# Kernel optimization log

Hardware: AMD Instinct MI355X
Metric: run time of the kernel (lower is better)

## Reference

```python
import jax, jax.numpy as jnp
import numpy as np

B, H, W, C = 2, 256, 256, 96
NH, WS, SS = 3, 8, 4
HD = C // NH
N = WS * WS              # tokens per window
NWIMG = (H // WS) * (W // WS)  # windows per image
MLP = 4 * C
EPS = 1e-5

def _np_attn_mask():
    img = np.zeros((H, W))
    sl = (slice(0, -WS), slice(-WS, -SS), slice(-SS, None))
    cnt = 0
    for a in sl:
        for b in sl:
            img[a, b] = cnt
            cnt += 1
    m = img.reshape(H // WS, WS, W // WS, WS).transpose(0, 2, 1, 3).reshape(-1, N)
    am = m[:, None, :] - m[:, :, None]
    return np.where(am != 0, -100.0, 0.0).astype(np.float32)

def _np_rel_index():
    coords = np.stack(np.meshgrid(np.arange(WS), np.arange(WS), indexing='ij'))
    cf = coords.reshape(2, -1)
    rel = (cf[:, :, None] - cf[:, None, :]).transpose(1, 2, 0).copy()
    rel[..., 0] += WS - 1
    rel[..., 1] += WS - 1
    rel[..., 0] *= 2 * WS - 1
    return rel.sum(-1)

def _np_coords_table():
    r = np.arange(-(WS - 1), WS, dtype=np.float32)
    t = np.stack(np.meshgrid(r, r, indexing='ij'), axis=-1) / (WS - 1) * 8.0
    t = np.sign(t) * np.log2(np.abs(t) + 1.0) / np.log2(8.0)
    return t.reshape(-1, 2)

ATTN_MASK = jnp.asarray(_np_attn_mask())          # [NWIMG, N, N]
REL_INDEX = jnp.asarray(_np_rel_index().reshape(-1))
COORDS_TABLE = jnp.asarray(_np_coords_table())    # [(2WS-1)^2, 2]

def setup_inputs():
    key = jax.random.key(0)
    ks = jax.random.split(key, 16)
    s = 0.02
    return {
        'hidden_states': jax.random.normal(ks[0], (B, H * W, C), jnp.float32),
        'time': jax.random.uniform(ks[1], (B,), jnp.float32),
        'q_w': jax.random.normal(ks[2], (C, C), jnp.float32) * s,
        'q_b': jnp.zeros((C,), jnp.float32),
        'k_w': jax.random.normal(ks[3], (C, C), jnp.float32) * s,
        'v_w': jax.random.normal(ks[4], (C, C), jnp.float32) * s,
        'v_b': jnp.zeros((C,), jnp.float32),
        'proj_w': jax.random.normal(ks[5], (C, C), jnp.float32) * s,
        'proj_b': jnp.zeros((C,), jnp.float32),
        'logit_scale': jnp.full((NH, 1, 1), jnp.log(10.0), jnp.float32),
        'cpb_w1': jax.random.normal(ks[6], (2, 512), jnp.float32) * s,
        'cpb_b1': jnp.zeros((512,), jnp.float32),
        'cpb_w2': jax.random.normal(ks[7], (512, NH), jnp.float32) * s,
        'lnb_ww': jax.random.normal(ks[8], (1, C), jnp.float32) * s,
        'lnb_wb': jnp.ones((C,), jnp.float32),
        'lnb_bw': jax.random.normal(ks[9], (1, C), jnp.float32) * s,
        'lnb_bb': jnp.zeros((C,), jnp.float32),
        'lna_ww': jax.random.normal(ks[10], (1, C), jnp.float32) * s,
        'lna_wb': jnp.ones((C,), jnp.float32),
        'lna_bw': jax.random.normal(ks[11], (1, C), jnp.float32) * s,
        'lna_bb': jnp.zeros((C,), jnp.float32),
        'fc1_w': jax.random.normal(ks[12], (C, MLP), jnp.float32) * s,
        'fc1_b': jnp.zeros((MLP,), jnp.float32),
        'fc2_w': jax.random.normal(ks[13], (MLP, C), jnp.float32) * s,
        'fc2_b': jnp.zeros((C,), jnp.float32),
    }

def _cln(x, time, ww, wb, bw, bb):
    # ConditionalLayerNorm: stats over channels, affine params from time via Linear(1, C)
    mean = x.mean(-1, keepdims=True)
    var = (x * x).mean(-1, keepdims=True) - mean * mean
    xn = (x - mean) / jnp.sqrt(var + EPS)
    t = time.reshape(-1, 1)
    w = (t @ ww + wb)[:, None, :]
    b = (t @ bw + bb)[:, None, :]
    return w * xn + b

def reference(hidden_states, time, q_w, q_b, k_w, v_w, v_b, proj_w, proj_b, logit_scale, cpb_w1, cpb_b1, cpb_w2, lnb_ww, lnb_wb, lnb_bw, lnb_bb, lna_ww, lna_wb, lna_bw, lna_bb, fc1_w, fc1_b, fc2_w, fc2_b):
    shortcut = hidden_states
    x = hidden_states.reshape(B, H, W, C)
    x = jnp.roll(x, (-SS, -SS), axis=(1, 2))  # cyclic shift
    # window partition -> [nW, N, C]
    xw = x.reshape(B, H // WS, WS, W // WS, WS, C).transpose(0, 1, 3, 2, 4, 5).reshape(-1, N, C)
    nW = B * NWIMG
    q = (xw @ q_w + q_b).reshape(nW, N, NH, HD).transpose(0, 2, 1, 3)
    k = (xw @ k_w).reshape(nW, N, NH, HD).transpose(0, 2, 1, 3)  # key has no bias in Swinv2
    v = (xw @ v_w + v_b).reshape(nW, N, NH, HD).transpose(0, 2, 1, 3)
    # cosine attention with clamped learnable log temperature
    qn = q / jnp.maximum(jnp.linalg.norm(q, axis=-1, keepdims=True), 1e-12)
    kn = k / jnp.maximum(jnp.linalg.norm(k, axis=-1, keepdims=True), 1e-12)
    scale = jnp.exp(jnp.minimum(logit_scale, jnp.log(100.0)))  # [NH,1,1]
    attn = jnp.einsum('whnd,whmd->whnm', qn, kn) * scale[None]
    # continuous relative position bias: MLP(2->512->NH) over log-spaced coords
    bias_table = jax.nn.relu(COORDS_TABLE @ cpb_w1 + cpb_b1) @ cpb_w2
    bias = bias_table[REL_INDEX].reshape(N, N, NH).transpose(2, 0, 1)
    attn = attn + 16.0 * jax.nn.sigmoid(bias)[None]
    # shifted-window mask
    attn = attn.reshape(B, NWIMG, NH, N, N) + ATTN_MASK[None, :, None]
    attn = jax.nn.softmax(attn.reshape(nW, NH, N, N), axis=-1)
    ctx = jnp.einsum('whnm,whmd->whnd', attn, v).transpose(0, 2, 1, 3).reshape(nW, N, C)
    ctx = ctx @ proj_w + proj_b
    # window reverse + un-shift
    xr = ctx.reshape(B, H // WS, W // WS, WS, WS, C).transpose(0, 1, 3, 2, 4, 5).reshape(B, H, W, C)
    xr = jnp.roll(xr, (SS, SS), axis=(1, 2))
    attn_out = xr.reshape(B, H * W, C)
    # post-norm residual (Swin v2 style) with conditional LN
    hs = shortcut + _cln(attn_out, time, lnb_ww, lnb_wb, lnb_bw, lnb_bb)
    inter = jax.nn.gelu(hs @ fc1_w + fc1_b, approximate=False)
    mlp_out = inter @ fc2_w + fc2_b
    return hs + _cln(mlp_out, time, lna_ww, lna_wb, lna_bw, lna_bb)
```

## Files before the change

kernel.cpp:

```cpp
#include <hip/hip_runtime.h>
#include <hip/hip_bf16.h>

typedef __bf16 bf16_t;
typedef bf16_t bf16x8 __attribute__((ext_vector_type(8)));
typedef bf16_t bf16x4 __attribute__((ext_vector_type(4)));
typedef float  f32x4  __attribute__((ext_vector_type(4)));

#define LDC 104
#define LDT 72
#define LDP 70
#define LDG 392

#define WS_WQ    0
#define WS_WK    19968
#define WS_WV    39936
#define WS_WP    59904
#define WS_FC1   79872
#define WS_FC2   159744
#define WS_BIAS  235008
#define WS_TBL   284160

__device__ __forceinline__ f32x4 mfma16(bf16x8 a, bf16x8 b, f32x4 c) {
    return __builtin_amdgcn_mfma_f32_16x16x32_bf16(a, b, c, 0, 0, 0);
}

__device__ __forceinline__ float cpbf(int v) {
    float x = (float)v * (8.0f / 7.0f);
    float l = log2f(fabsf(x) + 1.0f) * (1.0f / 3.0f);
    return x < 0.f ? -l : l;
}

__device__ __forceinline__ int regcnt(int t, int hw, int ww) {
    int r = t >> 3, c = t & 7;
    int rr = (hw == 31) ? (r < 4 ? 1 : 2) : 0;
    int cc = (ww == 31) ? (c < 4 ? 1 : 2) : 0;
    return rr * 3 + cc;
}

__global__ __launch_bounds__(256) void k0a_cpb(
    const float* __restrict__ cw1, const float* __restrict__ cb1,
    const float* __restrict__ cw2, char* __restrict__ ws)
{
    const int wv = threadIdx.x >> 6, lane = threadIdx.x & 63;
    const int e = blockIdx.x * 4 + wv;
    if (e >= 225) return;
    int ia = e / 15, ib = e % 15;
    float c0 = cpbf(ia - 7), c1 = cpbf(ib - 7);
    float a0 = 0.f, a1 = 0.f, a2 = 0.f;
    #pragma unroll
    for (int c = 0; c < 8; ++c) {
        int j = c * 64 + lane;
        float h = fmaf(c0, cw1[j], fmaf(c1, cw1[512 + j], cb1[j]));
        h = fmaxf(h, 0.f);
        a0 = fmaf(h, cw2[j * 3 + 0], a0);
        a1 = fmaf(h, cw2[j * 3 + 1], a1);
        a2 = fmaf(h, cw2[j * 3 + 2], a2);
    }
    #pragma unroll
    for (int m = 1; m < 64; m <<= 1) {
        a0 += __shfl_xor(a0, m);
        a1 += __shfl_xor(a1, m);
        a2 += __shfl_xor(a2, m);
    }
    if (lane == 0) {
        float* tbl = (float*)(ws + WS_TBL);
        tbl[e * 3 + 0] = a0; tbl[e * 3 + 1] = a1; tbl[e * 3 + 2] = a2;
    }
}

__global__ __launch_bounds__(512) void k0w_prep(
    const float* __restrict__ qw, const float* __restrict__ kw,
    const float* __restrict__ vw, const float* __restrict__ pw,
    const float* __restrict__ fc1w, const float* __restrict__ fc2w,
    char* __restrict__ ws)
{
    int tid = threadIdx.x;
    if (blockIdx.x < 54) {
        int rid = blockIdx.x * 512 + tid;
        if (rid < 9216) {
            int which = rid / 2304, r = rid % 2304;
            int i = r / 24, o4 = r % 24;
            const float* src = which == 0 ? qw : which == 1 ? kw : which == 2 ? vw : pw;
            float4 u = *(const float4*)(src + i * 96 + 4 * o4);
            bf16_t* dst = (bf16_t*)(ws + WS_WQ + which * 19968);
            dst[(4 * o4 + 0) * LDC + i] = (bf16_t)u.x;
            dst[(4 * o4 + 1) * LDC + i] = (bf16_t)u.y;
            dst[(4 * o4 + 2) * LDC + i] = (bf16_t)u.z;
            dst[(4 * o4 + 3) * LDC + i] = (bf16_t)u.w;
        } else if (rid < 18432) {
            int r = rid - 9216;
            int i = r / 96, m4 = r % 96;
            float4 u = *(const float4*)(fc1w + i * 384 + 4 * m4);
            bf16_t* dst = (bf16_t*)(ws + WS_FC1);
            dst[(4 * m4 + 0) * LDC + i] = (bf16_t)u.x;
            dst[(4 * m4 + 1) * LDC + i] = (bf16_t)u.y;
            dst[(4 * m4 + 2) * LDC + i] = (bf16_t)u.z;
            dst[(4 * m4 + 3) * LDC + i] = (bf16_t)u.w;
        } else {
            int r = rid - 18432;
            int g = r / 24, o4 = r % 24;
            float4 u = *(const float4*)(fc2w + g * 96 + 4 * o4);
            bf16_t* dst = (bf16_t*)(ws + WS_FC2);
            dst[(4 * o4 + 0) * LDG + g] = (bf16_t)u.x;
            dst[(4 * o4 + 1) * LDG + g] = (bf16_t)u.y;
            dst[(4 * o4 + 2) * LDG + g] = (bf16_t)u.z;
            dst[(4 * o4 + 3) * LDG + g] = (bf16_t)u.w;
        }
    } else {
        int e = (blockIdx.x - 54) * 512 + tid;
        if (e < 12288) {
            const float* tbl = (const float*)(ws + WS_TBL);
            float* bias = (float*)(ws + WS_BIAS);
            int h = e >> 12, nm = e & 4095, n = nm >> 6, m = nm & 63;
            int dr = (n >> 3) - (m >> 3) + 7, dc = (n & 7) - (m & 7) + 7;
            float t = tbl[(dr * 15 + dc) * 3 + h];
            bias[e] = 16.f / (1.f + __expf(-t));
        }
    }
}

__global__ __launch_bounds__(256, 3) void kA_attn(
    const float* __restrict__ hidden, const float* __restrict__ tv,
    const float* __restrict__ qb, const float* __restrict__ vb,
    const float* __restrict__ pb, const float* __restrict__ lsc,
    const float* __restrict__ lnww, const float* __restrict__ lnwb,
    const float* __restrict__ lnbw, const float* __restrict__ lnbb,
    const char* __restrict__ ws, float* __restrict__ hs)
{
    __shared__ __align__(16) char sm[40704];
    bf16_t* vT   = (bf16_t*)(sm + 0);
    bf16_t* qn   = (bf16_t*)(sm + 13824);
    bf16_t* kn   = (bf16_t*)(sm + 27136);
    bf16_t* P    = (bf16_t*)(sm + 13824);
    bf16_t* ctxb = (bf16_t*)(sm + 0);

    const int tid = threadIdx.x;
    const int wv = tid >> 6, lane = tid & 63, lg = lane >> 4, lr = lane & 15;
    const int wid = blockIdx.x;
    const int bat = wid >> 10, wim = wid & 1023, hw = wim >> 5, wwi = wim & 31;

    {
        bf16x8 af[3];
        {
            int tok = 16 * wv + lr;
            int gr = ((hw << 3) + (tok >> 3) + 4) & 255;
            int gc = ((wwi << 3) + (tok & 7) + 4) & 255;
            const float* xb = hidden + (((size_t)bat << 16) + (gr << 8) + gc) * 96;
            #pragma unroll
            for (int ks = 0; ks < 3; ++ks) {
                float4 u0 = *(const float4*)(xb + 32 * ks + 8 * lg);
                float4 u1 = *(const float4*)(xb + 32 * ks + 8 * lg + 4);
                bf16x8 f;
                f[0] = (bf16_t)u0.x; f[1] = (bf16_t)u0.y; f[2] = (bf16_t)u0.z; f[3] = (bf16_t)u0.w;
                f[4] = (bf16_t)u1.x; f[5] = (bf16_t)u1.y; f[6] = (bf16_t)u1.z; f[7] = (bf16_t)u1.w;
                af[ks] = f;
            }
        }
        const bf16_t* Wq = (const bf16_t*)(ws + WS_WQ);
        const bf16_t* Wk = (const bf16_t*)(ws + WS_WK);
        const bf16_t* Wv = (const bf16_t*)(ws + WS_WV);

        {
            bf16x8 wf[6][3];
            #pragma unroll
            for (int n = 0; n < 6; ++n)
                #pragma unroll
                for (int ks = 0; ks < 3; ++ks)
                    wf[n][ks] = *(const bf16x8*)(Wq + (16 * n + lr) * LDC + 32 * ks + 8 * lg);
            f32x4 acc[6];
            #pragma unroll
            for (int n = 0; n < 6; ++n) {
                f32x4 a = {0.f,0.f,0.f,0.f};
                #pragma unroll
                for (int ks = 0; ks < 3; ++ks) a = mfma16(af[ks], wf[n][ks], a);
                float bq = qb[16 * n + lr];
                #pragma unroll
                for (int j = 0; j < 4; ++j) a[j] += bq;
                acc[n] = a;
            }
            #pragma unroll
            for (int h = 0; h < 3; ++h)
                #pragma unroll
                for (int j = 0; j < 4; ++j) {
                    float s = acc[2*h][j] * acc[2*h][j] + acc[2*h+1][j] * acc[2*h+1][j];
                    s += __shfl_xor(s, 1); s += __shfl_xor(s, 2); s += __shfl_xor(s, 4); s += __shfl_xor(s, 8);
                    float inv = 1.f / fmaxf(sqrtf(s), 1e-12f);
                    int row = 16 * wv + 4 * lg + j;
                    qn[row * LDC + 32 * h + lr]      = (bf16_t)(acc[2*h][j] * inv);
                    qn[row * LDC + 32 * h + 16 + lr] = (bf16_t)(acc[2*h+1][j] * inv);
                }
        }
        {
            bf16x8 wf[6][3];
            #pragma unroll
            for (int n = 0; n < 6; ++n)
                #pragma unroll
                for (int ks = 0; ks < 3; ++ks)
                    wf[n][ks] = *(const bf16x8*)(Wk + (16 * n + lr) * LDC + 32 * ks + 8 * lg);
            f32x4 acc[6];
            #pragma unroll
            for (int n = 0; n < 6; ++n) {
                f32x4 a = {0.f,0.f,0.f,0.f};
                #pragma unroll
                for (int ks = 0; ks < 3; ++ks) a = mfma16(af[ks], wf[n][ks], a);
                acc[n] = a;
            }
            #pragma unroll
            for (int h = 0; h < 3; ++h)
                #pragma unroll
                for (int j = 0; j < 4; ++j) {
                    float s = acc[2*h][j] * acc[2*h][j] + acc[2*h+1][j] * acc[2*h+1][j];
                    s += __shfl_xor(s, 1); s += __shfl_xor(s, 2); s += __shfl_xor(s, 4); s += __shfl_xor(s, 8);
                    float inv = 1.f / fmaxf(sqrtf(s), 1e-12f);
                    int row = 16 * wv + 4 * lg + j;
                    kn[row * LDC + 32 * h + lr]      = (bf16_t)(acc[2*h][j] * inv);
                    kn[row * LDC + 32 * h + 16 + lr] = (bf16_t)(acc[2*h+1][j] * inv);
                }
        }
        {
            bf16x8 wf[6][3];
            #pragma unroll
            for (int n = 0; n < 6; ++n)
                #pragma unroll
                for (int ks = 0; ks < 3; ++ks)
                    wf[n][ks] = *(const bf16x8*)(Wv + (16 * n + lr) * LDC + 32 * ks + 8 * lg);
            #pragma unroll
            for (int n = 0; n < 6; ++n) {
                f32x4 a = {0.f,0.f,0.f,0.f};
                #pragma unroll
                for (int ks = 0; ks < 3; ++ks) a = mfma16(af[ks], wf[n][ks], a);
                float bv_ = vb[16 * n + lr];
                bf16x4 pk;
                #pragma unroll
                for (int j = 0; j < 4; ++j) pk[j] = (bf16_t)(a[j] + bv_);
                *(bf16x4*)(vT + (16 * n + lr) * LDT + 16 * wv + 4 * lg) = pk;
            }
        }
    }
    __syncthreads();

    {
        float br[3][4][4];
        const float* biasT = (const float*)(ws + WS_BIAS);
        #pragma unroll
        for (int h = 0; h < 3; ++h)
            #pragma unroll
            for (int f = 0; f < 4; ++f)
                #pragma unroll
                for (int j = 0; j < 4; ++j)
                    br[h][f][j] = biasT[(h << 12) + (16 * wv + 4 * lg + j) * 64 + 16 * f + lr];

        f32x4 s[3][4];
        #pragma unroll
        for (int h = 0; h < 3; ++h) {
            bf16x8 aq = *(const bf16x8*)(qn + (16 * wv + lr) * LDC + 32 * h + 8 * lg);
            bf16x8 bk[4];
            #pragma unroll
            for (int f = 0; f < 4; ++f)
                bk[f] = *(const bf16x8*)(kn + (16 * f + lr) * LDC + 32 * h + 8 * lg);
            #pragma unroll
            for (int f = 0; f < 4; ++f) {
                f32x4 z = {0.f,0.f,0.f,0.f};
                s[h][f] = mfma16(aq, bk[f], z);
            }
        }
        __syncthreads();

        float ls[3];
        #pragma unroll
        for (int h = 0; h < 3; ++h) ls[h] = __expf(fminf(lsc[h], 4.6051702f));
        int cntm[4], cnti[4];
        #pragma unroll
        for (int f = 0; f < 4; ++f) cntm[f] = regcnt(16 * f + lr, hw, wwi);
        #pragma unroll
        for (int j = 0; j < 4; ++j) cnti[j] = regcnt(16 * wv + 4 * lg + j, hw, wwi);
        #pragma unroll
        for (int h = 0; h < 3; ++h) {
            #pragma unroll
            for (int f = 0; f < 4; ++f)
                #pragma unroll
                for (int j = 0; j < 4; ++j) {
                    float mk = (cnti[j] != cntm[f]) ? -100.f : 0.f;
                    s[h][f][j] = fmaf(s[h][f][j], ls[h], br[h][f][j] + mk);
                }
            #pragma unroll
            for (int j = 0; j < 4; ++j) {
                float mx = fmaxf(fmaxf(s[h][0][j], s[h][1][j]), fmaxf(s[h][2][j], s[h][3][j]));
                mx = fmaxf(mx, __shfl_xor(mx, 1)); mx = fmaxf(mx, __shfl_xor(mx, 2));
                mx = fmaxf(mx, __shfl_xor(mx, 4)); mx = fmaxf(mx, __shfl_xor(mx, 8));
                float sum = 0.f;
                #pragma unroll
                for (int f = 0; f < 4; ++f) { float e = __expf(s[h][f][j] - mx); s[h][f][j] = e; sum += e; }
                sum += __shfl_xor(sum, 1); sum += __shfl_xor(sum, 2); sum += __shfl_xor(sum, 4); sum += __shfl_xor(sum, 8);
                float inv = 1.f / sum;
                int row = 16 * wv + 4 * lg + j;
                #pragma unroll
                for (int f = 0; f < 4; ++f)
                    P[h * 64 * LDP + row * LDP + 16 * f + lr] = (bf16_t)(s[h][f][j] * inv);
            }
        }
    }
    __syncthreads();

    {
        f32x4 ctx[6];
        #pragma unroll
        for (int t = 0; t < 6; ++t) { f32x4 z = {0.f,0.f,0.f,0.f}; ctx[t] = z; }
        bf16x8 ap[3][2], bv2[3][2][2];
        #pragma unroll
        for (int h = 0; h < 3; ++h)
            #pragma unroll
            for (int ks = 0; ks < 2; ++ks) {
                ap[h][ks] = *(const bf16x8*)(P + h * 64 * LDP + (16 * wv + lr) * LDP + 32 * ks + 8 * lg);
                #pragma unroll
                for (int dt = 0; dt < 2; ++dt)
                    bv2[h][dt][ks] = *(const bf16x8*)(vT + (32 * h + 16 * dt + lr) * LDT + 32 * ks + 8 * lg);
            }
        #pragma unroll
        for (int h = 0; h < 3; ++h)
            #pragma unroll
            for (int ks = 0; ks < 2; ++ks)
                #pragma unroll
                for (int dt = 0; dt < 2; ++dt)
                    ctx[2 * h + dt] = mfma16(ap[h][ks], bv2[h][dt][ks], ctx[2 * h + dt]);
        __syncthreads();
        #pragma unroll
        for (int t = 0; t < 6; ++t)
            #pragma unroll
            for (int j = 0; j < 4; ++j)
                ctxb[(16 * wv + 4 * lg + j) * LDC + 16 * t + lr] = (bf16_t)ctx[t][j];
    }
    __syncthreads();

    {
        const bf16_t* Wp = (const bf16_t*)(ws + WS_WP);
        bf16x8 wf[6][3];
        #pragma unroll
        for (int n = 0; n < 6; ++n)
            #pragma unroll
            for (int ks = 0; ks < 3; ++ks)
                wf[n][ks] = *(const bf16x8*)(Wp + (16 * n + lr) * LDC + 32 * ks + 8 * lg);
        bf16x8 af[3];
        #pragma unroll
        for (int ks = 0; ks < 3; ++ks) af[ks] = *(const bf16x8*)(ctxb + (16 * wv + lr) * LDC + 32 * ks + 8 * lg);
        f32x4 acc[6];
        #pragma unroll
        for (int n = 0; n < 6; ++n) {
            f32x4 a = {0.f,0.f,0.f,0.f};
            #pragma unroll
            for (int ks = 0; ks < 3; ++ks) a = mfma16(af[ks], wf[n][ks], a);
            float bp = pb[16 * n + lr];
            #pragma unroll
            for (int j = 0; j < 4; ++j) a[j] += bp;
            acc[n] = a;
        }
        float tb = tv[bat];
        float wco[6], bco[6];
        #pragma unroll
        for (int t = 0; t < 6; ++t) {
            int col = 16 * t + lr;
            wco[t] = fmaf(tb, lnww[col], lnwb[col]);
            bco[t] = fmaf(tb, lnbw[col], lnbb[col]);
        }
        #pragma unroll
        for (int j = 0; j < 4; ++j) {
            float smn = 0.f, sq = 0.f;
            #pragma unroll
            for (int t = 0; t < 6; ++t) { float v = acc[t][j]; smn += v; sq = fmaf(v, v, sq); }
            smn += __shfl_xor(smn, 1); smn += __shfl_xor(smn, 2); smn += __shfl_xor(smn, 4); smn += __shfl_xor(smn, 8);
            sq  += __shfl_xor(sq, 1);  sq  += __shfl_xor(sq, 2);  sq  += __shfl_xor(sq, 4);  sq  += __shfl_xor(sq, 8);
            float mean = smn * (1.f / 96.f);
            float var  = sq * (1.f / 96.f) - mean * mean;
            float rstd = rsqrtf(var + 1e-5f);
            int trow = 16 * wv + 4 * lg + j;
            int gr = ((hw << 3) + (trow >> 3) + 4) & 255;
            int gc = ((wwi << 3) + (trow & 7) + 4) & 255;
            size_t gbase = (((size_t)bat << 16) + (gr << 8) + gc) * 96;
            float hid[6];
            #pragma unroll
            for (int t = 0; t < 6; ++t) hid[t] = hidden[gbase + 16 * t + lr];
            #pragma unroll
            for (int t = 0; t < 6; ++t) {
                float xn = (acc[t][j] - mean) * rstd;
                hs[gbase + 16 * t + lr] = hid[t] + fmaf(wco[t], xn, bco[t]);
            }
        }
    }
}

__global__ __launch_bounds__(256, 3) void kB_mlp(
    const float* __restrict__ tv, const float* __restrict__ fc1b,
    const float* __restrict__ fc2b,
    const float* __restrict__ lnww, const float* __restrict__ lnwb,
    const float* __restrict__ lnbw, const float* __restrict__ lnbb,
    const char* __restrict__ ws, float* __restrict__ io)
{
    __shared__ __align__(16) bf16_t gbuf[64 * LDG];

    const int tid = threadIdx.x;
    const int wv = tid >> 6, lane = tid & 63, lg = lane >> 4, lr = lane & 15;
    const size_t t0 = (size_t)blockIdx.x * 64;

    bf16x8 hf[3];
    #pragma unroll
    for (int ks = 0; ks < 3; ++ks) {
        const float* p = io + (t0 + 16 * wv + lr) * 96 + 32 * ks + 8 * lg;
        float4 u0 = *(const float4*)p;
        float4 u1 = *(const float4*)(p + 4);
        bf16x8 f;
        f[0] = (bf16_t)u0.x; f[1] = (bf16_t)u0.y; f[2] = (bf16_t)u0.z; f[3] = (bf16_t)u0.w;
        f[4] = (bf16_t)u1.x; f[5] = (bf16_t)u1.y; f[6] = (bf16_t)u1.z; f[7] = (bf16_t)u1.w;
        hf[ks] = f;
    }

    const bf16_t* w1 = (const bf16_t*)(ws + WS_FC1);
    const bf16_t* w2 = (const bf16_t*)(ws + WS_FC2);

    #pragma unroll
    for (int g = 0; g < 4; ++g) {
        bf16x8 wf[6][3];
        #pragma unroll
        for (int n = 0; n < 6; ++n)
            #pragma unroll
            for (int ks = 0; ks < 3; ++ks)
                wf[n][ks] = *(const bf16x8*)(w1 + (16 * (6 * g + n) + lr) * LDC + 32 * ks + 8 * lg);
        #pragma unroll
        for (int n = 0; n < 6; ++n) {
            int nt = 6 * g + n;
            f32x4 a = {0.f,0.f,0.f,0.f};
            #pragma unroll
            for (int ks = 0; ks < 3; ++ks) a = mfma16(hf[ks], wf[n][ks], a);
            float bb = fc1b[16 * nt + lr];
            #pragma unroll
            for (int j = 0; j < 4; ++j) {
                float x = a[j] + bb;
                float u = 0.7978845608f * fmaf(0.044715f * x, x * x, x);
                float t = __expf(2.f * u);
                float g2 = x - x * __builtin_amdgcn_rcpf(t + 1.f);
                gbuf[(16 * wv + 4 * lg + j) * LDG + 16 * nt + lr] = (bf16_t)g2;
            }
        }
    }
    __syncthreads();

    f32x4 mlp[6];
    #pragma unroll
    for (int t = 0; t < 6; ++t) { f32x4 z = {0.f,0.f,0.f,0.f}; mlp[t] = z; }
    #pragma unroll
    for (int g = 0; g < 6; ++g) {
        bf16x8 gf[2], wf2[2][6];
        #pragma unroll
        for (int u = 0; u < 2; ++u) {
            int kk = 2 * g + u;
            gf[u] = *(const bf16x8*)(gbuf + (16 * wv + lr) * LDG + 32 * kk + 8 * lg);
            #pragma unroll
            for (int n = 0; n < 6; ++n)
                wf2[u][n] = *(const bf16x8*)(w2 + (16 * n + lr) * LDG + 32 * kk + 8 * lg);
        }
        #pragma unroll
        for (int u = 0; u < 2; ++u)
            #pragma unroll
            for (int n = 0; n < 6; ++n)
                mlp[n] = mfma16(gf[u], wf2[u][n], mlp[n]);
    }

    float tb = tv[t0 >> 16];
    float wco[6], bco[6];
    #pragma unroll
    for (int t = 0; t < 6; ++t) {
        int col = 16 * t + lr;
        wco[t] = fmaf(tb, lnww[col], lnwb[col]);
        bco[t] = fmaf(tb, lnbw[col], lnbb[col]);
        mlp[t][0] += fc2b[col]; mlp[t][1] += fc2b[col]; mlp[t][2] += fc2b[col]; mlp[t][3] += fc2b[col];
    }
    #pragma unroll
    for (int j = 0; j < 4; ++j) {
        float smn = 0.f, sq = 0.f;
        #pragma unroll
        for (int t = 0; t < 6; ++t) { float v = mlp[t][j]; smn += v; sq = fmaf(v, v, sq); }
        smn += __shfl_xor(smn, 1); smn += __shfl_xor(smn, 2); smn += __shfl_xor(smn, 4); smn += __shfl_xor(smn, 8);
        sq  += __shfl_xor(sq, 1);  sq  += __shfl_xor(sq, 2);  sq  += __shfl_xor(sq, 4);  sq  += __shfl_xor(sq, 8);
        float mean = smn * (1.f / 96.f);
        float var  = sq * (1.f / 96.f) - mean * mean;
        float rstd = rsqrtf(var + 1e-5f);
        size_t row = t0 + 16 * wv + 4 * lg + j;
        float hid[6];
        #pragma unroll
        for (int t = 0; t < 6; ++t) hid[t] = io[row * 96 + 16 * t + lr];
        #pragma unroll
        for (int t = 0; t < 6; ++t) {
            float xn = (mlp[t][j] - mean) * rstd;
            io[row * 96 + 16 * t + lr] = hid[t] + fmaf(wco[t], xn, bco[t]);
        }
    }
}

extern "C" void kernel_launch(void* const* d_in, const int* in_sizes, int n_in,
                              void* d_out, int out_size, void* d_ws, size_t ws_size,
                              hipStream_t stream)
{
    const float* hidden = (const float*)d_in[0];
    const float* tv     = (const float*)d_in[1];
    const float* q_w    = (const float*)d_in[2];
    const float* q_b    = (const float*)d_in[3];
    const float* k_w    = (const float*)d_in[4];
    const float* v_w    = (const float*)d_in[5];
    const float* v_b    = (const float*)d_in[6];
    const float* p_w    = (const float*)d_in[7];
    const float* p_b    = (const float*)d_in[8];
    const float* lsc    = (const float*)d_in[9];
    const float* cw1    = (const float*)d_in[10];
    const float* cb1    = (const float*)d_in[11];
    const float* cw2    = (const float*)d_in[12];
    const float* lnb_ww = (const float*)d_in[13];
    const float* lnb_wb = (const float*)d_in[14];
    const float* lnb_bw = (const float*)d_in[15];
    const float* lnb_bb = (const float*)d_in[16];
    const float* lna_ww = (const float*)d_in[17];
    const float* lna_wb = (const float*)d_in[18];
    const float* lna_bw = (const float*)d_in[19];
    const float* lna_bb = (const float*)d_in[20];
    const float* fc1_w  = (const float*)d_in[21];
    const float* fc1_b  = (const float*)d_in[22];
    const float* fc2_w  = (const float*)d_in[23];
    const float* fc2_b  = (const float*)d_in[24];
    char* ws = (char*)d_ws;
    float* out = (float*)d_out;

    k0a_cpb<<<dim3(57), dim3(256), 0, stream>>>(cw1, cb1, cw2, ws);
    k0w_prep<<<dim3(78), dim3(512), 0, stream>>>(q_w, k_w, v_w, p_w, fc1_w, fc2_w, ws);
    kA_attn<<<dim3(2048), dim3(256), 0, stream>>>(hidden, tv, q_b, v_b, p_b, lsc,
                                                  lnb_ww, lnb_wb, lnb_bw, lnb_bb, ws, out);
    kB_mlp<<<dim3(2048), dim3(256), 0, stream>>>(tv, fc1_b, fc2_b,
                                                 lna_ww, lna_wb, lna_bw, lna_bb, ws, out);
}
```

Before: 284.5 us.

## Stage MLP weights in LDS and keep GELU activations in registers via shuffles

The MLP kernel becomes a persistent-style kernel: 256 blocks of 512 threads each copy both bf16 weight matrices (fc1 and fc2, about 152 KB) into shared memory once. Each wave then handles four 16-token tiles. The products are transposed so the GELU outputs come out laid out for the second GEMM, and they are passed between lanes with shuffles instead of going through an LDS buffer. The attention bias table is also reordered so each thread reads its bias values with float4 loads. The cost is one LDS-resident block per CU and fewer blocks in flight, which may hurt latency hiding; the single 152 KB block per CU also means LDS capacity limits occupancy.

```diff
diff --git a/kernel.cpp b/kernel.cpp
--- a/kernel.cpp
+++ b/kernel.cpp
@@ -35,6 +35,12 @@
     int rr = (hw == 31) ? (r < 4 ? 1 : 2) : 0;
     int cc = (ww == 31) ? (c < 4 ? 1 : 2) : 0;
     return rr * 3 + cc;
+}
+
+__device__ __forceinline__ uint32_t pk2(float lo, float hi) {
+    union { bf16_t h[2]; uint32_t u; } z;
+    z.h[0] = (bf16_t)lo; z.h[1] = (bf16_t)hi;
+    return z.u;
 }
 
 __global__ __launch_bounds__(256) void k0a_cpb(
@@ -114,7 +120,7 @@
             int h = e >> 12, nm = e & 4095, n = nm >> 6, m = nm & 63;
             int dr = (n >> 3) - (m >> 3) + 7, dc = (n & 7) - (m & 7) + 7;
             float t = tbl[(dr * 15 + dc) * 3 + h];
-            bias[e] = 16.f / (1.f + __expf(-t));
+            bias[(h << 12) | (n << 6) | ((m & 15) << 2) | (m >> 4)] = 16.f / (1.f + __expf(-t));
         }
     }
 }
@@ -245,10 +251,10 @@
         #pragma unroll
         for (int h = 0; h < 3; ++h)
             #pragma unroll
-            for (int f = 0; f < 4; ++f)
-                #pragma unroll
-                for (int j = 0; j < 4; ++j)
-                    br[h][f][j] = biasT[(h << 12) + (16 * wv + 4 * lg + j) * 64 + 16 * f + lr];
+            for (int j = 0; j < 4; ++j) {
+                float4 u = *(const float4*)(biasT + (h << 12) + ((16 * wv + 4 * lg + j) << 6) + (lr << 2));
+                br[h][0][j] = u.x; br[h][1][j] = u.y; br[h][2][j] = u.z; br[h][3][j] = u.w;
+            }
 
         f32x4 s[3][4];
         #pragma unroll
@@ -388,109 +394,169 @@
     }
 }
 
-__global__ __launch_bounds__(256, 3) void kB_mlp(
+__global__ __launch_bounds__(512, 2) void kB_mlp(
     const float* __restrict__ tv, const float* __restrict__ fc1b,
     const float* __restrict__ fc2b,
     const float* __restrict__ lnww, const float* __restrict__ lnwb,
     const float* __restrict__ lnbw, const float* __restrict__ lnbb,
     const char* __restrict__ ws, float* __restrict__ io)
 {
-    __shared__ __align__(16) bf16_t gbuf[64 * LDG];
-
+    __shared__ __align__(16) char smem[155648];
     const int tid = threadIdx.x;
-    const int wv = tid >> 6, lane = tid & 63, lg = lane >> 4, lr = lane & 15;
-    const size_t t0 = (size_t)blockIdx.x * 64;
-
-    bf16x8 hf[3];
-    #pragma unroll
-    for (int ks = 0; ks < 3; ++ks) {
-        const float* p = io + (t0 + 16 * wv + lr) * 96 + 32 * ks + 8 * lg;
-        float4 u0 = *(const float4*)p;
-        float4 u1 = *(const float4*)(p + 4);
-        bf16x8 f;
-        f[0] = (bf16_t)u0.x; f[1] = (bf16_t)u0.y; f[2] = (bf16_t)u0.z; f[3] = (bf16_t)u0.w;
-        f[4] = (bf16_t)u1.x; f[5] = (bf16_t)u1.y; f[6] = (bf16_t)u1.z; f[7] = (bf16_t)u1.w;
-        hf[ks] = f;
-    }
-
-    const bf16_t* w1 = (const bf16_t*)(ws + WS_FC1);
-    const bf16_t* w2 = (const bf16_t*)(ws + WS_FC2);
-
-    #pragma unroll
-    for (int g = 0; g < 4; ++g) {
-        bf16x8 wf[6][3];
-        #pragma unroll
-        for (int n = 0; n < 6; ++n)
-            #pragma unroll
-            for (int ks = 0; ks < 3; ++ks)
-                wf[n][ks] = *(const bf16x8*)(w1 + (16 * (6 * g + n) + lr) * LDC + 32 * ks + 8 * lg);
-        #pragma unroll
-        for (int n = 0; n < 6; ++n) {
-            int nt = 6 * g + n;
-            f32x4 a = {0.f,0.f,0.f,0.f};
-            #pragma unroll
-            for (int ks = 0; ks < 3; ++ks) a = mfma16(hf[ks], wf[n][ks], a);
-            float bb = fc1b[16 * nt + lr];
-            #pragma unroll
-            for (int j = 0; j < 4; ++j) {
-                float x = a[j] + bb;
-                float u = 0.7978845608f * fmaf(0.044715f * x, x * x, x);
-                float t = __expf(2.f * u);
-                float g2 = x - x * __builtin_amdgcn_rcpf(t + 1.f);
-                gbuf[(16 * wv + 4 * lg + j) * LDG + 16 * nt + lr] = (bf16_t)g2;
-            }
+    const int wv = tid >> 6, lane = tid & 63;
+    const int lg = (lane >> 4) & 3, lr = lane & 15;
+
+    {
+        const float4* src = (const float4*)(ws + WS_FC1);
+        float4* dst = (float4*)smem;
+        #pragma unroll
+        for (int r = 0; r < 19; ++r) {
+            int idx = tid + 512 * r;
+            dst[idx] = src[idx];
         }
     }
     __syncthreads();
 
-    f32x4 mlp[6];
-    #pragma unroll
-    for (int t = 0; t < 6; ++t) { f32x4 z = {0.f,0.f,0.f,0.f}; mlp[t] = z; }
-    #pragma unroll
-    for (int g = 0; g < 6; ++g) {
-        bf16x8 gf[2], wf2[2][6];
-        #pragma unroll
-        for (int u = 0; u < 2; ++u) {
-            int kk = 2 * g + u;
-            gf[u] = *(const bf16x8*)(gbuf + (16 * wv + lr) * LDG + 32 * kk + 8 * lg);
-            #pragma unroll
-            for (int n = 0; n < 6; ++n)
-                wf2[u][n] = *(const bf16x8*)(w2 + (16 * n + lr) * LDG + 32 * kk + 8 * lg);
-        }
-        #pragma unroll
-        for (int u = 0; u < 2; ++u)
-            #pragma unroll
-            for (int n = 0; n < 6; ++n)
-                mlp[n] = mfma16(gf[u], wf2[u][n], mlp[n]);
-    }
-
-    float tb = tv[t0 >> 16];
-    float wco[6], bco[6];
-    #pragma unroll
-    for (int t = 0; t < 6; ++t) {
-        int col = 16 * t + lr;
-        wco[t] = fmaf(tb, lnww[col], lnwb[col]);
-        bco[t] = fmaf(tb, lnbw[col], lnbb[col]);
-        mlp[t][0] += fc2b[col]; mlp[t][1] += fc2b[col]; mlp[t][2] += fc2b[col]; mlp[t][3] += fc2b[col];
-    }
-    #pragma unroll
-    for (int j = 0; j < 4; ++j) {
-        float smn = 0.f, sq = 0.f;
-        #pragma unroll
-        for (int t = 0; t < 6; ++t) { float v = mlp[t][j]; smn += v; sq = fmaf(v, v, sq); }
-        smn += __shfl_xor(smn, 1); smn += __shfl_xor(smn, 2); smn += __shfl_xor(smn, 4); smn += __shfl_xor(smn, 8);
-        sq  += __shfl_xor(sq, 1);  sq  += __shfl_xor(sq, 2);  sq  += __shfl_xor(sq, 4);  sq  += __shfl_xor(sq, 8);
-        float mean = smn * (1.f / 96.f);
-        float var  = sq * (1.f / 96.f) - mean * mean;
-        float rstd = rsqrtf(var + 1e-5f);
-        size_t row = t0 + 16 * wv + 4 * lg + j;
-        float hid[6];
-        #pragma unroll
-        for (int t = 0; t < 6; ++t) hid[t] = io[row * 96 + 16 * t + lr];
-        #pragma unroll
-        for (int t = 0; t < 6; ++t) {
-            float xn = (mlp[t][j] - mean) * rstd;
-            io[row * 96 + 16 * t + lr] = hid[t] + fmaf(wco[t], xn, bco[t]);
+    const bf16_t* w1 = (const bf16_t*)smem;
+    const bf16_t* w2 = (const bf16_t*)(smem + 79872);
+
+    #pragma unroll 1
+    for (int pass = 0; pass < 2; ++pass) {
+        const int tA = blockIdx.x * 32 + wv * 4 + pass * 2;
+
+        bf16x8 hf[2][3];
+        float tb[2];
+        #pragma unroll
+        for (int p = 0; p < 2; ++p) {
+            const int t0 = (tA + p) * 16;
+            tb[p] = tv[(tA + p) >> 12];
+            const float* hb = io + (size_t)(t0 + lr) * 96;
+            #pragma unroll
+            for (int ks = 0; ks < 3; ++ks) {
+                float4 u0 = *(const float4*)(hb + 32 * ks + 8 * lg);
+                float4 u1 = *(const float4*)(hb + 32 * ks + 8 * lg + 4);
+                bf16x8 f;
+                f[0] = (bf16_t)u0.x; f[1] = (bf16_t)u0.y; f[2] = (bf16_t)u0.z; f[3] = (bf16_t)u0.w;
+                f[4] = (bf16_t)u1.x; f[5] = (bf16_t)u1.y; f[6] = (bf16_t)u1.z; f[7] = (bf16_t)u1.w;
+                hf[p][ks] = f;
+            }
+        }
+
+        f32x4 mlp[2][6];
+        #pragma unroll
+        for (int p = 0; p < 2; ++p)
+            #pragma unroll
+            for (int t = 0; t < 6; ++t) { f32x4 z = {0.f,0.f,0.f,0.f}; mlp[p][t] = z; }
+
+        #pragma unroll
+        for (int ch = 0; ch < 4; ++ch) {
+            f32x4 acc[2][6];
+            #pragma unroll
+            for (int half = 0; half < 2; ++half) {
+                bf16x8 a1[3][3];
+                #pragma unroll
+                for (int n2 = 0; n2 < 3; ++n2)
+                    #pragma unroll
+                    for (int ks = 0; ks < 3; ++ks)
+                        a1[n2][ks] = *(const bf16x8*)(w1 + (96 * ch + 16 * (3 * half + n2) + lr) * LDC + 32 * ks + 8 * lg);
+                #pragma unroll
+                for (int p = 0; p < 2; ++p)
+                    #pragma unroll
+                    for (int n2 = 0; n2 < 3; ++n2) {
+                        f32x4 a = {0.f,0.f,0.f,0.f};
+                        #pragma unroll
+                        for (int ks = 0; ks < 3; ++ks) a = mfma16(a1[n2][ks], hf[p][ks], a);
+                        acc[p][3 * half + n2] = a;
+                    }
+            }
+            uint32_t P0[2][6], P1[2][6];
+            #pragma unroll
+            for (int nt = 0; nt < 6; ++nt) {
+                float4 b4 = *(const float4*)(fc1b + 96 * ch + 16 * nt + 4 * lg);
+                #pragma unroll
+                for (int p = 0; p < 2; ++p) {
+                    float g_[4];
+                    #pragma unroll
+                    for (int j = 0; j < 4; ++j) {
+                        float x = acc[p][nt][j] + ((const float*)&b4)[j];
+                        float u = 0.7978845608f * fmaf(0.044715f * x, x * x, x);
+                        float t = __expf(2.f * u);
+                        g_[j] = x - x * __builtin_amdgcn_rcpf(t + 1.f);
+                    }
+                    P0[p][nt] = pk2(g_[0], g_[1]);
+                    P1[p][nt] = pk2(g_[2], g_[3]);
+                }
+            }
+            const int s01 = lr + 32 * (lg & 1);
+            const int s23 = s01 + 16;
+            const bool hi = lg >= 2;
+            #pragma unroll
+            for (int kk = 0; kk < 3; ++kk) {
+                int kkg = 3 * ch + kk;
+                bf16x8 a2[6];
+                #pragma unroll
+                for (int ot = 0; ot < 6; ++ot)
+                    a2[ot] = *(const bf16x8*)(w2 + (16 * ot + lr) * LDG + 32 * kkg + 8 * lg);
+                #pragma unroll
+                for (int p = 0; p < 2; ++p) {
+                    uint32_t A0 = __shfl((int)P0[p][2*kk],   s01);
+                    uint32_t A1 = __shfl((int)P1[p][2*kk],   s01);
+                    uint32_t A2 = __shfl((int)P0[p][2*kk],   s23);
+                    uint32_t A3 = __shfl((int)P1[p][2*kk],   s23);
+                    uint32_t B0 = __shfl((int)P0[p][2*kk+1], s01);
+                    uint32_t B1 = __shfl((int)P1[p][2*kk+1], s01);
+                    uint32_t B2 = __shfl((int)P0[p][2*kk+1], s23);
+                    uint32_t B3 = __shfl((int)P1[p][2*kk+1], s23);
+                    union { uint32_t w[4]; bf16x8 v; } gg;
+                    gg.w[0] = hi ? B0 : A0;
+                    gg.w[1] = hi ? B1 : A1;
+                    gg.w[2] = hi ? B2 : A2;
+                    gg.w[3] = hi ? B3 : A3;
+                    #pragma unroll
+                    for (int ot = 0; ot < 6; ++ot)
+                        mlp[p][ot] = mfma16(a2[ot], gg.v, mlp[p][ot]);
+                }
+            }
+        }
+
+        #pragma unroll
+        for (int p = 0; p < 2; ++p) {
+            const int t0 = (tA + p) * 16;
+            #pragma unroll
+            for (int ot = 0; ot < 6; ++ot) {
+                float4 b2 = *(const float4*)(fc2b + 16 * ot + 4 * lg);
+                #pragma unroll
+                for (int j = 0; j < 4; ++j) mlp[p][ot][j] += ((const float*)&b2)[j];
+            }
+            float smn = 0.f, sq = 0.f;
+            #pragma unroll
+            for (int ot = 0; ot < 6; ++ot)
+                #pragma unroll
+                for (int j = 0; j < 4; ++j) { float v = mlp[p][ot][j]; smn += v; sq = fmaf(v, v, sq); }
+            smn += __shfl_xor(smn, 16); smn += __shfl_xor(smn, 32);
+            sq  += __shfl_xor(sq, 16);  sq  += __shfl_xor(sq, 32);
+            float mean = smn * (1.f / 96.f);
+            float var  = sq * (1.f / 96.f) - mean * mean;
+            float rstd = rsqrtf(var + 1e-5f);
+
+            float* rowp = io + (size_t)(t0 + lr) * 96;
+            #pragma unroll
+            for (int ot = 0; ot < 6; ++ot) {
+                float4 ww_ = *(const float4*)(lnww + 16 * ot + 4 * lg);
+                float4 wb_ = *(const float4*)(lnwb + 16 * ot + 4 * lg);
+                float4 bw_ = *(const float4*)(lnbw + 16 * ot + 4 * lg);
+                float4 bb_ = *(const float4*)(lnbb + 16 * ot + 4 * lg);
+                float4 hid = *(const float4*)(rowp + 16 * ot + 4 * lg);
+                float4 o;
+                #pragma unroll
+                for (int j = 0; j < 4; ++j) {
+                    float w = fmaf(tb[p], ((const float*)&ww_)[j], ((const float*)&wb_)[j]);
+                    float b = fmaf(tb[p], ((const float*)&bw_)[j], ((const float*)&bb_)[j]);
+                    float xn = (mlp[p][ot][j] - mean) * rstd;
+                    ((float*)&o)[j] = ((const float*)&hid)[j] + fmaf(w, xn, b);
+                }
+                *(float4*)(rowp + 16 * ot + 4 * lg) = o;
+            }
         }
     }
 }
@@ -531,6 +597,6 @@
     k0w_prep<<<dim3(78), dim3(512), 0, stream>>>(q_w, k_w, v_w, p_w, fc1_w, fc2_w, ws);
     kA_attn<<<dim3(2048), dim3(256), 0, stream>>>(hidden, tv, q_b, v_b, p_b, lsc,
                                                   lnb_ww, lnb_wb, lnb_bw, lnb_bb, ws, out);
-    kB_mlp<<<dim3(2048), dim3(256), 0, stream>>>(tv, fc1_b, fc2_b,
-                                                 lna_ww, lna_wb, lna_bw, lna_bb, ws, out);
-}
+    kB_mlp<<<dim3(256), dim3(512), 0, stream>>>(tv, fc1_b, fc2_b,
+                                                lna_ww, lna_wb, lna_bw, lna_bb, ws, out);
+}
```

Measured after the change: 468.8 us. 1.65x slower.

## Stage MLP weights in LDS per hidden chunk and double tokens per block

Applied to the files above, without the earlier changes.

The MLP kernel now handles 128 tokens per block and walks the 384-wide hidden dimension in four chunks of 96. For each chunk it copies the fc1 and fc2 weight slices into shared memory and computes GELU into a small LDS buffer. The partial fc2 products accumulate in registers, which replaces the per-wave global weight loads and the large full-width GELU buffer. Separately, the relative-position bias table is stored permuted so the attention kernel reads it with float4 loads. The cost is more shared memory (occupancy hint dropped to 2), extra barriers per chunk, and half as many blocks.

```diff
diff --git a/kernel.cpp b/kernel.cpp
--- a/kernel.cpp
+++ b/kernel.cpp
@@ -7,18 +7,18 @@
 typedef float  f32x4  __attribute__((ext_vector_type(4)));
 
 #define LDC 104
+#define LDW 100
 #define LDT 72
 #define LDP 70
-#define LDG 392
 
 #define WS_WQ    0
 #define WS_WK    19968
 #define WS_WV    39936
 #define WS_WP    59904
 #define WS_FC1   79872
-#define WS_FC2   159744
-#define WS_BIAS  235008
-#define WS_TBL   284160
+#define WS_FC2   156672
+#define WS_BIAS  233472
+#define WS_TBL   282624
 
 __device__ __forceinline__ f32x4 mfma16(bf16x8 a, bf16x8 b, f32x4 c) {
     return __builtin_amdgcn_mfma_f32_16x16x32_bf16(a, b, c, 0, 0, 0);
@@ -92,19 +92,20 @@
             int i = r / 96, m4 = r % 96;
             float4 u = *(const float4*)(fc1w + i * 384 + 4 * m4);
             bf16_t* dst = (bf16_t*)(ws + WS_FC1);
-            dst[(4 * m4 + 0) * LDC + i] = (bf16_t)u.x;
-            dst[(4 * m4 + 1) * LDC + i] = (bf16_t)u.y;
-            dst[(4 * m4 + 2) * LDC + i] = (bf16_t)u.z;
-            dst[(4 * m4 + 3) * LDC + i] = (bf16_t)u.w;
+            dst[(4 * m4 + 0) * LDW + i] = (bf16_t)u.x;
+            dst[(4 * m4 + 1) * LDW + i] = (bf16_t)u.y;
+            dst[(4 * m4 + 2) * LDW + i] = (bf16_t)u.z;
+            dst[(4 * m4 + 3) * LDW + i] = (bf16_t)u.w;
         } else {
             int r = rid - 18432;
             int g = r / 24, o4 = r % 24;
+            int ch = g / 96, m = g % 96;
             float4 u = *(const float4*)(fc2w + g * 96 + 4 * o4);
             bf16_t* dst = (bf16_t*)(ws + WS_FC2);
-            dst[(4 * o4 + 0) * LDG + g] = (bf16_t)u.x;
-            dst[(4 * o4 + 1) * LDG + g] = (bf16_t)u.y;
-            dst[(4 * o4 + 2) * LDG + g] = (bf16_t)u.z;
-            dst[(4 * o4 + 3) * LDG + g] = (bf16_t)u.w;
+            dst[(ch * 96 + 4 * o4 + 0) * LDW + m] = (bf16_t)u.x;
+            dst[(ch * 96 + 4 * o4 + 1) * LDW + m] = (bf16_t)u.y;
+            dst[(ch * 96 + 4 * o4 + 2) * LDW + m] = (bf16_t)u.z;
+            dst[(ch * 96 + 4 * o4 + 3) * LDW + m] = (bf16_t)u.w;
         }
     } else {
         int e = (blockIdx.x - 54) * 512 + tid;
@@ -114,7 +115,7 @@
             int h = e >> 12, nm = e & 4095, n = nm >> 6, m = nm & 63;
             int dr = (n >> 3) - (m >> 3) + 7, dc = (n & 7) - (m & 7) + 7;
             float t = tbl[(dr * 15 + dc) * 3 + h];
-            bias[e] = 16.f / (1.f + __expf(-t));
+            bias[(h << 12) | (n << 6) | ((m & 15) << 2) | (m >> 4)] = 16.f / (1.f + __expf(-t));
         }
     }
 }
@@ -245,10 +246,10 @@
         #pragma unroll
         for (int h = 0; h < 3; ++h)
             #pragma unroll
-            for (int f = 0; f < 4; ++f)
-                #pragma unroll
-                for (int j = 0; j < 4; ++j)
-                    br[h][f][j] = biasT[(h << 12) + (16 * wv + 4 * lg + j) * 64 + 16 * f + lr];
+            for (int j = 0; j < 4; ++j) {
+                float4 u = *(const float4*)(biasT + (h << 12) + ((16 * wv + 4 * lg + j) << 6) + (lr << 2));
+                br[h][0][j] = u.x; br[h][1][j] = u.y; br[h][2][j] = u.z; br[h][3][j] = u.w;
+            }
 
         f32x4 s[3][4];
         #pragma unroll
@@ -388,109 +389,139 @@
     }
 }
 
-__global__ __launch_bounds__(256, 3) void kB_mlp(
+__global__ __launch_bounds__(256, 2) void kB_mlp(
     const float* __restrict__ tv, const float* __restrict__ fc1b,
     const float* __restrict__ fc2b,
     const float* __restrict__ lnww, const float* __restrict__ lnwb,
     const float* __restrict__ lnbw, const float* __restrict__ lnbb,
     const char* __restrict__ ws, float* __restrict__ io)
 {
-    __shared__ __align__(16) bf16_t gbuf[64 * LDG];
+    __shared__ __align__(16) char smem[65024];
+    bf16_t* w1c  = (bf16_t*)(smem + 0);
+    bf16_t* w2c  = (bf16_t*)(smem + 19200);
+    bf16_t* gbuf = (bf16_t*)(smem + 38400);
 
     const int tid = threadIdx.x;
     const int wv = tid >> 6, lane = tid & 63, lg = lane >> 4, lr = lane & 15;
-    const size_t t0 = (size_t)blockIdx.x * 64;
-
-    bf16x8 hf[3];
+    const int tblk = blockIdx.x * 128;
+    const float tb = tv[tblk >> 16];
+
+    bf16x8 af[2][3];
     #pragma unroll
-    for (int ks = 0; ks < 3; ++ks) {
-        const float* p = io + (t0 + 16 * wv + lr) * 96 + 32 * ks + 8 * lg;
-        float4 u0 = *(const float4*)p;
-        float4 u1 = *(const float4*)(p + 4);
-        bf16x8 f;
-        f[0] = (bf16_t)u0.x; f[1] = (bf16_t)u0.y; f[2] = (bf16_t)u0.z; f[3] = (bf16_t)u0.w;
-        f[4] = (bf16_t)u1.x; f[5] = (bf16_t)u1.y; f[6] = (bf16_t)u1.z; f[7] = (bf16_t)u1.w;
-        hf[ks] = f;
-    }
-
-    const bf16_t* w1 = (const bf16_t*)(ws + WS_FC1);
-    const bf16_t* w2 = (const bf16_t*)(ws + WS_FC2);
-
+    for (int mt = 0; mt < 2; ++mt) {
+        const float* hb = io + (size_t)(tblk + 32 * wv + 16 * mt + lr) * 96;
+        #pragma unroll
+        for (int ks = 0; ks < 3; ++ks) {
+            float4 u0 = *(const float4*)(hb + 32 * ks + 8 * lg);
+            float4 u1 = *(const float4*)(hb + 32 * ks + 8 * lg + 4);
+            bf16x8 f;
+            f[0] = (bf16_t)u0.x; f[1] = (bf16_t)u0.y; f[2] = (bf16_t)u0.z; f[3] = (bf16_t)u0.w;
+            f[4] = (bf16_t)u1.x; f[5] = (bf16_t)u1.y; f[6] = (bf16_t)u1.z; f[7] = (bf16_t)u1.w;
+            af[mt][ks] = f;
+        }
+    }
+
+    f32x4 mlp[2][6];
     #pragma unroll
-    for (int g = 0; g < 4; ++g) {
-        bf16x8 wf[6][3];
-        #pragma unroll
-        for (int n = 0; n < 6; ++n)
+    for (int mt = 0; mt < 2; ++mt)
+        #pragma unroll
+        for (int ot = 0; ot < 6; ++ot) { f32x4 z = {0.f,0.f,0.f,0.f}; mlp[mt][ot] = z; }
+
+    #pragma unroll 1
+    for (int ch = 0; ch < 4; ++ch) {
+        if (ch) __syncthreads();
+        {
+            const float4* s1 = (const float4*)(ws + WS_FC1 + ch * 19200);
+            const float4* s2 = (const float4*)(ws + WS_FC2 + ch * 19200);
+            float4* d1 = (float4*)w1c;
+            float4* d2 = (float4*)w2c;
+            #pragma unroll
+            for (int i = 0; i < 5; ++i) {
+                int idx = tid + 256 * i;
+                if (idx < 1200) { d1[idx] = s1[idx]; d2[idx] = s2[idx]; }
+            }
+        }
+        __syncthreads();
+
+        #pragma unroll
+        for (int nt = 0; nt < 6; ++nt) {
+            bf16x8 b1[3];
             #pragma unroll
             for (int ks = 0; ks < 3; ++ks)
-                wf[n][ks] = *(const bf16x8*)(w1 + (16 * (6 * g + n) + lr) * LDC + 32 * ks + 8 * lg);
-        #pragma unroll
-        for (int n = 0; n < 6; ++n) {
-            int nt = 6 * g + n;
-            f32x4 a = {0.f,0.f,0.f,0.f};
-            #pragma unroll
-            for (int ks = 0; ks < 3; ++ks) a = mfma16(hf[ks], wf[n][ks], a);
-            float bb = fc1b[16 * nt + lr];
-            #pragma unroll
-            for (int j = 0; j < 4; ++j) {
-                float x = a[j] + bb;
-                float u = 0.7978845608f * fmaf(0.044715f * x, x * x, x);
-                float t = __expf(2.f * u);
-                float g2 = x - x * __builtin_amdgcn_rcpf(t + 1.f);
-                gbuf[(16 * wv + 4 * lg + j) * LDG + 16 * nt + lr] = (bf16_t)g2;
-            }
-        }
-    }
-    __syncthreads();
-
-    f32x4 mlp[6];
-    #pragma unroll
-    for (int t = 0; t < 6; ++t) { f32x4 z = {0.f,0.f,0.f,0.f}; mlp[t] = z; }
-    #pragma unroll
-    for (int g = 0; g < 6; ++g) {
-        bf16x8 gf[2], wf2[2][6];
-        #pragma unroll
-        for (int u = 0; u < 2; ++u) {
-            int kk = 2 * g + u;
-            gf[u] = *(const bf16x8*)(gbuf + (16 * wv + lr) * LDG + 32 * kk + 8 * lg);
-            #pragma unroll
-            for (int n = 0; n < 6; ++n)
-                wf2[u][n] = *(const bf16x8*)(w2 + (16 * n + lr) * LDG + 32 * kk + 8 * lg);
-        }
-        #pragma unroll
-        for (int u = 0; u < 2; ++u)
-            #pragma unroll
-            for (int n = 0; n < 6; ++n)
-                mlp[n] = mfma16(gf[u], wf2[u][n], mlp[n]);
-    }
-
-    float tb = tv[t0 >> 16];
+                b1[ks] = *(const bf16x8*)(w1c + (16 * nt + lr) * LDW + 32 * ks + 8 * lg);
+            float bb = fc1b[96 * ch + 16 * nt + lr];
+            #pragma unroll
+            for (int mt = 0; mt < 2; ++mt) {
+                f32x4 a = {0.f,0.f,0.f,0.f};
+                #pragma unroll
+                for (int ks = 0; ks < 3; ++ks) a = mfma16(af[mt][ks], b1[ks], a);
+                #pragma unroll
+                for (int j = 0; j < 4; ++j) {
+                    float x = a[j] + bb;
+                    float u = 0.7978845608f * fmaf(0.044715f * x, x * x, x);
+                    float t = __expf(2.f * u);
+                    float g = x - x * __builtin_amdgcn_rcpf(t + 1.f);
+                    gbuf[(32 * wv + 16 * mt + 4 * lg + j) * LDC + 16 * nt + lr] = (bf16_t)g;
+                }
+            }
+        }
+        __syncthreads();
+
+        #pragma unroll
+        for (int kk = 0; kk < 3; ++kk) {
+            bf16x8 gf[2];
+            #pragma unroll
+            for (int mt = 0; mt < 2; ++mt)
+                gf[mt] = *(const bf16x8*)(gbuf + (32 * wv + 16 * mt + lr) * LDC + 32 * kk + 8 * lg);
+            #pragma unroll
+            for (int oh = 0; oh < 2; ++oh) {
+                bf16x8 a2[3];
+                #pragma unroll
+                for (int o3 = 0; o3 < 3; ++o3)
+                    a2[o3] = *(const bf16x8*)(w2c + (16 * (3 * oh + o3) + lr) * LDW + 32 * kk + 8 * lg);
+                #pragma unroll
+                for (int mt = 0; mt < 2; ++mt)
+                    #pragma unroll
+                    for (int o3 = 0; o3 < 3; ++o3)
+                        mlp[mt][3 * oh + o3] = mfma16(gf[mt], a2[o3], mlp[mt][3 * oh + o3]);
+            }
+        }
+    }
+
     float wco[6], bco[6];
     #pragma unroll
-    for (int t = 0; t < 6; ++t) {
-        int col = 16 * t + lr;
-        wco[t] = fmaf(tb, lnww[col], lnwb[col]);
-        bco[t] = fmaf(tb, lnbw[col], lnbb[col]);
-        mlp[t][0] += fc2b[col]; mlp[t][1] += fc2b[col]; mlp[t][2] += fc2b[col]; mlp[t][3] += fc2b[col];
+    for (int ot = 0; ot < 6; ++ot) {
+        int col = 16 * ot + lr;
+        wco[ot] = fmaf(tb, lnww[col], lnwb[col]);
+        bco[ot] = fmaf(tb, lnbw[col], lnbb[col]);
     }
     #pragma unroll
-    for (int j = 0; j < 4; ++j) {
-        float smn = 0.f, sq = 0.f;
-        #pragma unroll
-        for (int t = 0; t < 6; ++t) { float v = mlp[t][j]; smn += v; sq = fmaf(v, v, sq); }
-        smn += __shfl_xor(smn, 1); smn += __shfl_xor(smn, 2); smn += __shfl_xor(smn, 4); smn += __shfl_xor(smn, 8);
-        sq  += __shfl_xor(sq, 1);  sq  += __shfl_xor(sq, 2);  sq  += __shfl_xor(sq, 4);  sq  += __shfl_xor(sq, 8);
-        float mean = smn * (1.f / 96.f);
-        float var  = sq * (1.f / 96.f) - mean * mean;
-        float rstd = rsqrtf(var + 1e-5f);
-        size_t row = t0 + 16 * wv + 4 * lg + j;
-        float hid[6];
-        #pragma unroll
-        for (int t = 0; t < 6; ++t) hid[t] = io[row * 96 + 16 * t + lr];
-        #pragma unroll
-        for (int t = 0; t < 6; ++t) {
-            float xn = (mlp[t][j] - mean) * rstd;
-            io[row * 96 + 16 * t + lr] = hid[t] + fmaf(wco[t], xn, bco[t]);
+    for (int mt = 0; mt < 2; ++mt) {
+        #pragma unroll
+        for (int ot = 0; ot < 6; ++ot) {
+            float bb = fc2b[16 * ot + lr];
+            #pragma unroll
+            for (int j = 0; j < 4; ++j) mlp[mt][ot][j] += bb;
+        }
+        #pragma unroll
+        for (int j = 0; j < 4; ++j) {
+            float smn = 0.f, sq = 0.f;
+            #pragma unroll
+            for (int ot = 0; ot < 6; ++ot) { float v = mlp[mt][ot][j]; smn += v; sq = fmaf(v, v, sq); }
+            smn += __shfl_xor(smn, 1); smn += __shfl_xor(smn, 2); smn += __shfl_xor(smn, 4); smn += __shfl_xor(smn, 8);
+            sq  += __shfl_xor(sq, 1);  sq  += __shfl_xor(sq, 2);  sq  += __shfl_xor(sq, 4);  sq  += __shfl_xor(sq, 8);
+            float mean = smn * (1.f / 96.f);
+            float var  = sq * (1.f / 96.f) - mean * mean;
+            float rstd = rsqrtf(var + 1e-5f);
+            size_t row = (size_t)tblk + 32 * wv + 16 * mt + 4 * lg + j;
+            float hid[6];
+            #pragma unroll
+            for (int ot = 0; ot < 6; ++ot) hid[ot] = io[row * 96 + 16 * ot + lr];
+            #pragma unroll
+            for (int ot = 0; ot < 6; ++ot) {
+                float xn = (mlp[mt][ot][j] - mean) * rstd;
+                io[row * 96 + 16 * ot + lr] = hid[ot] + fmaf(wco[ot], xn, bco[ot]);
+            }
         }
     }
 }
@@ -531,6 +562,6 @@
     k0w_prep<<<dim3(78), dim3(512), 0, stream>>>(q_w, k_w, v_w, p_w, fc1_w, fc2_w, ws);
     kA_attn<<<dim3(2048), dim3(256), 0, stream>>>(hidden, tv, q_b, v_b, p_b, lsc,
                                                   lnb_ww, lnb_wb, lnb_bw, lnb_bb, ws, out);
-    kB_mlp<<<dim3(2048), dim3(256), 0, stream>>>(tv, fc1_b, fc2_b,
+    kB_mlp<<<dim3(1024), dim3(256), 0, stream>>>(tv, fc1_b, fc2_b,
                                                  lna_ww, lna_wb, lna_bw, lna_bb, ws, out);
 }
```

Result: slower. 293.3 us (+3.1%).
